# Performance work log

Hardware: AMD Instinct MI355X
Metric: run time of the kernel (lower is better)

The kernel has to match this reference:

```python
import jax, jax.numpy as jnp
import numpy as np

B, N, C = 4, 2048, 320
H, D = 5, 64            # heads, dim_head
INNER = H * D           # 320


def setup_inputs() -> dict:
    key = jax.random.key(0)
    ks = jax.random.split(key, 7)
    x = jax.random.normal(ks[0], (B, N, C), dtype=jnp.float32)
    edge = jax.random.uniform(ks[1], (B, N, 1), dtype=jnp.float32)
    s = 1.0 / np.sqrt(C)
    Wq = jax.random.normal(ks[2], (C, INNER), dtype=jnp.float32) * s
    Wk = jax.random.normal(ks[3], (C, INNER), dtype=jnp.float32) * s
    Wv = jax.random.normal(ks[4], (C, INNER), dtype=jnp.float32) * s
    Wo = jax.random.normal(ks[5], (INNER, C), dtype=jnp.float32) * (1.0 / np.sqrt(INNER))
    bo = jnp.zeros((C,), dtype=jnp.float32)
    return {"x": x, "edge": edge, "Wq": Wq, "Wk": Wk, "Wv": Wv, "Wo": Wo, "bo": bo}


def _split_heads(t):
    # 'b n (h d) -> (b h) n d'  (batch-major, head-minor)
    b, n, _ = t.shape
    return t.reshape(b, n, H, D).transpose(0, 2, 1, 3).reshape(b * H, n, D)


def reference(x, edge, Wq, Wk, Wv, Wo, bo):
    scale = D ** -0.5
    q = _split_heads(x @ Wq).astype(jnp.float32)   # (B*H, N, D)
    k = _split_heads(x @ Wk).astype(jnp.float32)
    v = _split_heads(x @ Wv)

    sim = jnp.einsum('bid,bjd->bij', q, k) * scale  # (B*H, N, N)

    # torch: edge.repeat(h, 1, 1) -> batch-minor tiling; index i uses edge[i % B]
    edge_rep = jnp.tile(edge, (H, 1, 1))            # (H*B, N, 1)
    edge_matrix = edge_rep * edge_rep.transpose(0, 2, 1)  # outer product (H*B, N, N)

    sim = jax.nn.softmax(sim * edge_matrix, axis=-1)
    out = jnp.einsum('bij,bjd->bid', sim, v)        # (B*H, N, D)

    # '(b h) n d -> b n (h d)'
    out = out.reshape(B, H, N, D).transpose(0, 2, 1, 3).reshape(B, N, INNER)
    return out @ Wo + bo
```

## Files before the change

### kernel.cpp

```cpp
#include <hip/hip_runtime.h>
#include <hip/hip_bf16.h>
#include <math.h>


typedef short bf16x8 __attribute__((ext_vector_type(8)));
typedef float f32x4 __attribute__((ext_vector_type(4)));

static __device__ __forceinline__ ushort f2bf(float f) {
  union { float f; unsigned u; } v; v.f = f;
  unsigned r = (v.u + 0x7fffu + ((v.u >> 16) & 1u)) >> 16;
  return (ushort)r;
}
static __device__ __forceinline__ float fexp2(float x) {
#if __has_builtin(__builtin_amdgcn_exp2f)
  return __builtin_amdgcn_exp2f(x);
#else
  return exp2f(x);
#endif
}
static __device__ __forceinline__ f32x4 mfma32(bf16x8 a, bf16x8 b, f32x4 c) {
  return __builtin_amdgcn_mfma_f32_16x16x32_bf16(a, b, c, 0, 0, 0);
}

#define GLD_LDS16(gsrc, ldst)                                                  \
  __builtin_amdgcn_global_load_lds(                                            \
      (const __attribute__((address_space(1))) unsigned int*)(gsrc),           \
      (__attribute__((address_space(3))) unsigned int*)(ldst), 16, 0, 0)

__global__ __launch_bounds__(256) void prep_kernel(
    const float* __restrict__ x,
    const float* __restrict__ Wq, const float* __restrict__ Wk,
    const float* __restrict__ Wv, const float* __restrict__ Wo,
    ushort* __restrict__ xb, ushort* __restrict__ wt)
{
  const int w = blockIdx.x;
  if (w < 2560) {
    const int t = threadIdx.x;
    const int mt2 = w / 5;
    const int kc = (w % 5) * 2 + (t >> 7);
    const int f = (t & 127) * 4;
    const int qq = f >> 7, mm = (f >> 3) & 15, e0 = f & 7;
    float4 v = *reinterpret_cast<const float4*>(
        x + (size_t)(mt2 * 16 + mm) * 320 + kc * 32 + qq * 8 + e0);
    ushort4 o = { f2bf(v.x), f2bf(v.y), f2bf(v.z), f2bf(v.w) };
    *reinterpret_cast<ushort4*>(xb + (size_t)(mt2 * 10 + kc) * 512 + f) = o;
  } else {
    const int w2 = w - 2560;
    const int nt2 = w2 % 20, kc = (w2 / 20) % 10, z = w2 / 200;
    const float* W = z == 0 ? Wq : z == 1 ? Wk : z == 2 ? Wv : Wo;
    const int f = threadIdx.x * 2;
    const int qq = f >> 7, nn = (f >> 3) & 15, e0 = f & 7;
    const int k = kc * 32 + qq * 8 + e0, n = nt2 * 16 + nn;
    float v0 = W[(size_t)k * 320 + n];
    float v1 = W[(size_t)(k + 1) * 320 + n];
    ushort2 o = { f2bf(v0), f2bf(v1) };
    *reinterpret_cast<ushort2*>(
        wt + (size_t)z * 102400 + (size_t)(nt2 * 10 + kc) * 512 + f) = o;
  }
}

__global__ __launch_bounds__(256, 3) void qkv_gemm(
    const ushort* __restrict__ xb, const float* __restrict__ edge,
    const ushort* __restrict__ wt,
    ushort* __restrict__ qp, ushort* __restrict__ kS, ushort* __restrict__ vS)
{
  const int w = blockIdx.x;
  const int s = (w & 7) * 60 + (w >> 3);
  const int mg = s / 15, zh = s % 15;
  const int z = zh / 5, h = zh % 5;
  const int wave = threadIdx.x >> 6, lane = threadIdx.x & 63;
  const int m16 = lane & 15, quad = lane >> 4;
  const int m0 = mg * 256 + wave * 64;
  const ushort* atile = xb + (size_t)(m0 >> 4) * 5120 + lane * 8;
  const ushort* btile = wt + (size_t)z * 102400 + (size_t)(h * 4) * 5120 + lane * 8;

  f32x4 acc[4][4];
#pragma unroll
  for (int i = 0; i < 4; ++i)
#pragma unroll
    for (int ns = 0; ns < 4; ++ns) acc[i][ns] = (f32x4){0.f, 0.f, 0.f, 0.f};

#pragma unroll
  for (int kc = 0; kc < 10; ++kc) {
    bf16x8 af[4], bf[4];
#pragma unroll
    for (int i = 0; i < 4; ++i)
      af[i] = *reinterpret_cast<const bf16x8*>(atile + (i * 10 + kc) * 512);
#pragma unroll
    for (int ns = 0; ns < 4; ++ns)
      bf[ns] = *reinterpret_cast<const bf16x8*>(btile + (ns * 10 + kc) * 512);
    if (z == 2) {
#pragma unroll
      for (int i = 0; i < 4; ++i)
#pragma unroll
        for (int ns = 0; ns < 4; ++ns)
          acc[i][ns] = mfma32(af[i], bf[ns], acc[i][ns]);
    } else {
#pragma unroll
      for (int i = 0; i < 4; ++i)
#pragma unroll
        for (int ns = 0; ns < 4; ++ns)
          acc[i][ns] = mfma32(bf[ns], af[i], acc[i][ns]);
    }
  }

  const float QSCALE = 0.18033688011112042f;
  const int b = m0 >> 11;
  const int bh = b * 5 + h;
  const float* eb = edge + (size_t)((b + h) & 3) * 2048;
  const int nwb = m0 & 2047;

  if (z == 0) {
#pragma unroll
    for (int i = 0; i < 4; ++i) {
      const int n = nwb + i * 16 + m16;
      const float e = eb[n] * QSCALE;
      ushort* dst = qp + ((size_t)bh * 2048 + n) * 64 + quad * 4;
#pragma unroll
      for (int ns = 0; ns < 4; ++ns) {
        ushort4 o = { f2bf(acc[i][ns][0] * e), f2bf(acc[i][ns][1] * e),
                      f2bf(acc[i][ns][2] * e), f2bf(acc[i][ns][3] * e) };
        *reinterpret_cast<ushort4*>(dst + ns * 16) = o;
      }
    }
  } else if (z == 1) {
#pragma unroll
    for (int i = 0; i < 4; ++i) {
      const int j = nwb + i * 16 + m16;
      const float e = eb[j];
      const size_t base = (size_t)bh * 131072 +
                          (size_t)((m0 >> 4) + i & 127) * 1024;
#pragma unroll
      for (int ns = 0; ns < 4; ++ns) {
        size_t a0 = base + (ns >> 1) * 512 +
                    ((((ns * 2 + (quad >> 1)) & 3) * 16 + m16)) * 8 +
                    (quad & 1) * 4;
        ushort4 o = { f2bf(acc[i][ns][0] * e), f2bf(acc[i][ns][1] * e),
                      f2bf(acc[i][ns][2] * e), f2bf(acc[i][ns][3] * e) };
        *reinterpret_cast<ushort4*>(kS + a0) = o;
      }
    }
  } else {
    const int jb = nwb >> 6;
#pragma unroll
    for (int i = 0; i < 4; ++i) {
      const int kb = i >> 1, e4 = (i & 1) * 4;
#pragma unroll
      for (int ns = 0; ns < 4; ++ns) {
        ushort4 o = { f2bf(acc[i][ns][0]), f2bf(acc[i][ns][1]),
                      f2bf(acc[i][ns][2]), f2bf(acc[i][ns][3]) };
        size_t addr = (size_t)bh * 131072 + (size_t)ns * 32768 +
                      (size_t)jb * 1024 + kb * 512 +
                      (quad * 16 + m16) * 8 + e4;
        *reinterpret_cast<ushort4*>(vS + addr) = o;
      }
    }
  }
}

__global__ __launch_bounds__(256, 4) void attn_kernel(
    const ushort* __restrict__ qp, const ushort* __restrict__ kS,
    const ushort* __restrict__ vS, ushort* __restrict__ ao)
{
  __shared__ ushort sm[16384];
  const int w = blockIdx.x;
  const int s = (w & 7) * 80 + (w >> 3);
  const int bh = s >> 5, qt = s & 31;
  const int b = bh / 5, h = bh % 5;
  const int wave = threadIdx.x >> 6, lane = threadIdx.x & 63;
  const int m16 = lane & 15, quad = lane >> 4;
  const int q0 = qt * 64;

  bf16x8 qf[2];
  {
    const ushort* qrow = qp + ((size_t)bh * 2048 + q0 + wave * 16 + m16) * 64;
    qf[0] = *reinterpret_cast<const bf16x8*>(qrow + quad * 8);
    qf[1] = *reinterpret_cast<const bf16x8*>(qrow + 32 + quad * 8);
  }

  const ushort* kbase = kS + (size_t)bh * 131072;
  const ushort* vbase = vS + (size_t)bh * 131072;

  f32x4 oacc[4];
  float rs = 0.f;
#pragma unroll
  for (int dt = 0; dt < 4; ++dt) oacc[dt] = (f32x4){0.f, 0.f, 0.f, 0.f};

  auto stage = [&](int jt, int buf) {
    const ushort* ks = kbase + (size_t)jt * 4096 + wave * 1024 + lane * 8;
    const ushort* vs = vbase + (size_t)wave * 32768 + (size_t)jt * 1024 + lane * 8;
    ushort* dk = &sm[buf * 8192 + wave * 1024];
    ushort* dv = &sm[buf * 8192 + 4096 + wave * 1024];
#pragma unroll
    for (int is = 0; is < 2; ++is) {
      GLD_LDS16(ks + is * 512, dk + is * 512);
      GLD_LDS16(vs + is * 512, dv + is * 512);
    }
  };

  stage(0, 0);
  __syncthreads();

  int cur = 0;
  for (int jt = 0; jt < 32; ++jt) {
    if (jt < 31) stage(jt + 1, cur ^ 1);
    const ushort* kb0 = &sm[cur * 8192];
    const ushort* vb0 = &sm[cur * 8192 + 4096];
#pragma unroll
    for (int uu = 0; uu < 2; ++uu) {
      bf16x8 kf[2][2], vf[4];
#pragma unroll
      for (int ss = 0; ss < 2; ++ss)
#pragma unroll
        for (int hf = 0; hf < 2; ++hf)
          kf[ss][hf] = *reinterpret_cast<const bf16x8*>(
              kb0 + uu * 2048 + ss * 1024 + hf * 512 + lane * 8);
#pragma unroll
      for (int dt = 0; dt < 4; ++dt)
        vf[dt] = *reinterpret_cast<const bf16x8*>(
            vb0 + dt * 1024 + uu * 512 + lane * 8);

      f32x4 st0 = (f32x4){0.f, 0.f, 0.f, 0.f};
      f32x4 st1 = (f32x4){0.f, 0.f, 0.f, 0.f};
      st0 = mfma32(kf[0][0], qf[0], st0);
      st0 = mfma32(kf[0][1], qf[1], st0);
      st1 = mfma32(kf[1][0], qf[0], st1);
      st1 = mfma32(kf[1][1], qf[1], st1);
      unsigned b0 = __float_as_uint(fexp2(st0[0]));
      unsigned b1 = __float_as_uint(fexp2(st0[1]));
      unsigned b2 = __float_as_uint(fexp2(st0[2]));
      unsigned b3 = __float_as_uint(fexp2(st0[3]));
      unsigned b4 = __float_as_uint(fexp2(st1[0]));
      unsigned b5 = __float_as_uint(fexp2(st1[1]));
      unsigned b6 = __float_as_uint(fexp2(st1[2]));
      unsigned b7 = __float_as_uint(fexp2(st1[3]));
      float t0 = __uint_as_float(b0 & 0xffff0000u);
      float t1 = __uint_as_float(b1 & 0xffff0000u);
      float t2 = __uint_as_float(b2 & 0xffff0000u);
      float t3 = __uint_as_float(b3 & 0xffff0000u);
      float t4 = __uint_as_float(b4 & 0xffff0000u);
      float t5 = __uint_as_float(b5 & 0xffff0000u);
      float t6 = __uint_as_float(b6 & 0xffff0000u);
      float t7 = __uint_as_float(b7 & 0xffff0000u);
      rs += ((t0 + t1) + (t2 + t3)) + ((t4 + t5) + (t6 + t7));
      union { unsigned u[4]; bf16x8 v; } pk;
      pk.u[0] = __builtin_amdgcn_perm(b1, b0, 0x07060302u);
      pk.u[1] = __builtin_amdgcn_perm(b3, b2, 0x07060302u);
      pk.u[2] = __builtin_amdgcn_perm(b5, b4, 0x07060302u);
      pk.u[3] = __builtin_amdgcn_perm(b7, b6, 0x07060302u);
#pragma unroll
      for (int dt = 0; dt < 4; ++dt)
        oacc[dt] = mfma32(vf[dt], pk.v, oacc[dt]);
    }
    __syncthreads();
    cur ^= 1;
  }

  rs += __shfl_xor(rs, 16, 64);
  rs += __shfl_xor(rs, 32, 64);
  const float inv = 1.0f / rs;

  const int mt2 = b * 128 + qt * 4 + wave;
#pragma unroll
  for (int dt = 0; dt < 4; ++dt) {
    f32x4 a = oacc[dt];
    unsigned r0 = f2bf(a[0] * inv), r1 = f2bf(a[1] * inv);
    unsigned r2 = f2bf(a[2] * inv), r3 = f2bf(a[3] * inv);
    uint2 ww;
    ww.x = r0 | (r1 << 16);
    ww.y = r2 | (r3 << 16);
    size_t addr = (size_t)(mt2 * 10 + h * 2 + (dt >> 1)) * 512 +
                  ((((dt & 1) * 2 + (quad >> 1)) * 16 + m16)) * 8 +
                  (quad & 1) * 4;
    *reinterpret_cast<uint2*>(ao + addr) = ww;
  }
}

__global__ __launch_bounds__(256, 3) void oproj_gemm(
    const ushort* __restrict__ ao, const ushort* __restrict__ wt,
    const float* __restrict__ bo, float* __restrict__ out)
{
  const int w = blockIdx.x;
  const int s = (w & 7) * 40 + (w >> 3);
  const int mg = s / 5, ct = s % 5;
  const int wave = threadIdx.x >> 6, lane = threadIdx.x & 63;
  const int m16 = lane & 15, quad = lane >> 4;
  const int m0 = mg * 128 + wave * 32;
  const int n0 = ct * 64;
  const ushort* atile = ao + (size_t)(m0 >> 4) * 5120 + lane * 8;
  const ushort* btile = wt + (size_t)3 * 102400 + (size_t)(ct * 4) * 5120 + lane * 8;

  f32x4 acc[2][4];
#pragma unroll
  for (int i = 0; i < 2; ++i)
#pragma unroll
    for (int ns = 0; ns < 4; ++ns) acc[i][ns] = (f32x4){0.f, 0.f, 0.f, 0.f};

#pragma unroll
  for (int kc = 0; kc < 10; ++kc) {
    bf16x8 af[2], bf[4];
#pragma unroll
    for (int i = 0; i < 2; ++i)
      af[i] = *reinterpret_cast<const bf16x8*>(atile + (i * 10 + kc) * 512);
#pragma unroll
    for (int ns = 0; ns < 4; ++ns)
      bf[ns] = *reinterpret_cast<const bf16x8*>(btile + (ns * 10 + kc) * 512);
#pragma unroll
    for (int i = 0; i < 2; ++i)
#pragma unroll
      for (int ns = 0; ns < 4; ++ns)
        acc[i][ns] = mfma32(bf[ns], af[i], acc[i][ns]);
  }

  float4 bb[4];
#pragma unroll
  for (int ns = 0; ns < 4; ++ns)
    bb[ns] = *reinterpret_cast<const float4*>(bo + n0 + ns * 16 + quad * 4);
#pragma unroll
  for (int i = 0; i < 2; ++i) {
    const int mrow = m0 + i * 16 + m16;
#pragma unroll
    for (int ns = 0; ns < 4; ++ns) {
      float4 o;
      o.x = acc[i][ns][0] + bb[ns].x;
      o.y = acc[i][ns][1] + bb[ns].y;
      o.z = acc[i][ns][2] + bb[ns].z;
      o.w = acc[i][ns][3] + bb[ns].w;
      *reinterpret_cast<float4*>(
          out + (size_t)mrow * 320 + n0 + ns * 16 + quad * 4) = o;
    }
  }
}

extern "C" void kernel_launch(void* const* d_in, const int* in_sizes, int n_in,
                              void* d_out, int out_size, void* d_ws, size_t ws_size,
                              hipStream_t stream) {
  const float* x    = (const float*)d_in[0];
  const float* edge = (const float*)d_in[1];
  const float* Wq   = (const float*)d_in[2];
  const float* Wk   = (const float*)d_in[3];
  const float* Wv   = (const float*)d_in[4];
  const float* Wo   = (const float*)d_in[5];
  const float* bo   = (const float*)d_in[6];
  float* out = (float*)d_out;

  ushort* xb = (ushort*)d_ws;
  ushort* wt = xb + (size_t)8192 * 320;
  ushort* qp = wt + (size_t)4 * 320 * 320;
  ushort* kS = qp + (size_t)20 * 2048 * 64;
  ushort* vS = kS + (size_t)20 * 2048 * 64;
  ushort* ao = vS + (size_t)20 * 2048 * 64;

  prep_kernel<<<3360, 256, 0, stream>>>(x, Wq, Wk, Wv, Wo, xb, wt);
  qkv_gemm<<<480, 256, 0, stream>>>(xb, edge, wt, qp, kS, vS);
  attn_kernel<<<640, 256, 0, stream>>>(qp, kS, vS, ao);
  oproj_gemm<<<320, 256, 0, stream>>>(ao, wt, bo, out);
}
```

Before: 128.1 us.

## Process two query tiles per wave to reuse staged K/V across more queries

Each wave in the attention kernel now computes two 16-row query subtiles, so a block covers 128 queries instead of 64 and the grid is halved. K/V tiles loaded into shared memory and the K/V fragments read from it are reused for twice the query work. This cuts global K/V traffic and LDS reads per query, at the cost of more accumulator registers and fewer blocks, which may unbalance CU occupancy.

```diff
diff --git a/kernel.cpp b/kernel.cpp
--- a/kernel.cpp
+++ b/kernel.cpp
@@ -164,27 +164,31 @@
 {
   __shared__ ushort sm[16384];
   const int w = blockIdx.x;
-  const int s = (w & 7) * 80 + (w >> 3);
-  const int bh = s >> 5, qt = s & 31;
+  const int s = (w & 7) * 40 + (w >> 3);
+  const int bh = s >> 4, qt = s & 15;
   const int b = bh / 5, h = bh % 5;
   const int wave = threadIdx.x >> 6, lane = threadIdx.x & 63;
   const int m16 = lane & 15, quad = lane >> 4;
-  const int q0 = qt * 64;
-
-  bf16x8 qf[2];
-  {
-    const ushort* qrow = qp + ((size_t)bh * 2048 + q0 + wave * 16 + m16) * 64;
-    qf[0] = *reinterpret_cast<const bf16x8*>(qrow + quad * 8);
-    qf[1] = *reinterpret_cast<const bf16x8*>(qrow + 32 + quad * 8);
+  const int q0 = qt * 128;
+
+  bf16x8 qf[2][2];
+#pragma unroll
+  for (int qt2 = 0; qt2 < 2; ++qt2) {
+    const ushort* qrow =
+        qp + ((size_t)bh * 2048 + q0 + wave * 32 + qt2 * 16 + m16) * 64;
+    qf[qt2][0] = *reinterpret_cast<const bf16x8*>(qrow + quad * 8);
+    qf[qt2][1] = *reinterpret_cast<const bf16x8*>(qrow + 32 + quad * 8);
   }
 
   const ushort* kbase = kS + (size_t)bh * 131072;
   const ushort* vbase = vS + (size_t)bh * 131072;
 
-  f32x4 oacc[4];
-  float rs = 0.f;
-#pragma unroll
-  for (int dt = 0; dt < 4; ++dt) oacc[dt] = (f32x4){0.f, 0.f, 0.f, 0.f};
+  f32x4 oacc[2][4];
+  float rs[2] = {0.f, 0.f};
+#pragma unroll
+  for (int qt2 = 0; qt2 < 2; ++qt2)
+#pragma unroll
+    for (int dt = 0; dt < 4; ++dt) oacc[qt2][dt] = (f32x4){0.f, 0.f, 0.f, 0.f};
 
   auto stage = [&](int jt, int buf) {
     const ushort* ks = kbase + (size_t)jt * 4096 + wave * 1024 + lane * 8;
@@ -220,59 +224,66 @@
         vf[dt] = *reinterpret_cast<const bf16x8*>(
             vb0 + dt * 1024 + uu * 512 + lane * 8);
 
-      f32x4 st0 = (f32x4){0.f, 0.f, 0.f, 0.f};
-      f32x4 st1 = (f32x4){0.f, 0.f, 0.f, 0.f};
-      st0 = mfma32(kf[0][0], qf[0], st0);
-      st0 = mfma32(kf[0][1], qf[1], st0);
-      st1 = mfma32(kf[1][0], qf[0], st1);
-      st1 = mfma32(kf[1][1], qf[1], st1);
-      unsigned b0 = __float_as_uint(fexp2(st0[0]));
-      unsigned b1 = __float_as_uint(fexp2(st0[1]));
-      unsigned b2 = __float_as_uint(fexp2(st0[2]));
-      unsigned b3 = __float_as_uint(fexp2(st0[3]));
-      unsigned b4 = __float_as_uint(fexp2(st1[0]));
-      unsigned b5 = __float_as_uint(fexp2(st1[1]));
-      unsigned b6 = __float_as_uint(fexp2(st1[2]));
-      unsigned b7 = __float_as_uint(fexp2(st1[3]));
-      float t0 = __uint_as_float(b0 & 0xffff0000u);
-      float t1 = __uint_as_float(b1 & 0xffff0000u);
-      float t2 = __uint_as_float(b2 & 0xffff0000u);
-      float t3 = __uint_as_float(b3 & 0xffff0000u);
-      float t4 = __uint_as_float(b4 & 0xffff0000u);
-      float t5 = __uint_as_float(b5 & 0xffff0000u);
-      float t6 = __uint_as_float(b6 & 0xffff0000u);
-      float t7 = __uint_as_float(b7 & 0xffff0000u);
-      rs += ((t0 + t1) + (t2 + t3)) + ((t4 + t5) + (t6 + t7));
-      union { unsigned u[4]; bf16x8 v; } pk;
-      pk.u[0] = __builtin_amdgcn_perm(b1, b0, 0x07060302u);
-      pk.u[1] = __builtin_amdgcn_perm(b3, b2, 0x07060302u);
-      pk.u[2] = __builtin_amdgcn_perm(b5, b4, 0x07060302u);
-      pk.u[3] = __builtin_amdgcn_perm(b7, b6, 0x07060302u);
-#pragma unroll
-      for (int dt = 0; dt < 4; ++dt)
-        oacc[dt] = mfma32(vf[dt], pk.v, oacc[dt]);
+#pragma unroll
+      for (int qt2 = 0; qt2 < 2; ++qt2) {
+        f32x4 st0 = (f32x4){0.f, 0.f, 0.f, 0.f};
+        f32x4 st1 = (f32x4){0.f, 0.f, 0.f, 0.f};
+        st0 = mfma32(kf[0][0], qf[qt2][0], st0);
+        st0 = mfma32(kf[0][1], qf[qt2][1], st0);
+        st1 = mfma32(kf[1][0], qf[qt2][0], st1);
+        st1 = mfma32(kf[1][1], qf[qt2][1], st1);
+        unsigned b0 = __float_as_uint(fexp2(st0[0]));
+        unsigned b1 = __float_as_uint(fexp2(st0[1]));
+        unsigned b2 = __float_as_uint(fexp2(st0[2]));
+        unsigned b3 = __float_as_uint(fexp2(st0[3]));
+        unsigned b4 = __float_as_uint(fexp2(st1[0]));
+        unsigned b5 = __float_as_uint(fexp2(st1[1]));
+        unsigned b6 = __float_as_uint(fexp2(st1[2]));
+        unsigned b7 = __float_as_uint(fexp2(st1[3]));
+        float t0 = __uint_as_float(b0 & 0xffff0000u);
+        float t1 = __uint_as_float(b1 & 0xffff0000u);
+        float t2 = __uint_as_float(b2 & 0xffff0000u);
+        float t3 = __uint_as_float(b3 & 0xffff0000u);
+        float t4 = __uint_as_float(b4 & 0xffff0000u);
+        float t5 = __uint_as_float(b5 & 0xffff0000u);
+        float t6 = __uint_as_float(b6 & 0xffff0000u);
+        float t7 = __uint_as_float(b7 & 0xffff0000u);
+        rs[qt2] += ((t0 + t1) + (t2 + t3)) + ((t4 + t5) + (t6 + t7));
+        union { unsigned u[4]; bf16x8 v; } pk;
+        pk.u[0] = __builtin_amdgcn_perm(b1, b0, 0x07060302u);
+        pk.u[1] = __builtin_amdgcn_perm(b3, b2, 0x07060302u);
+        pk.u[2] = __builtin_amdgcn_perm(b5, b4, 0x07060302u);
+        pk.u[3] = __builtin_amdgcn_perm(b7, b6, 0x07060302u);
+#pragma unroll
+        for (int dt = 0; dt < 4; ++dt)
+          oacc[qt2][dt] = mfma32(vf[dt], pk.v, oacc[qt2][dt]);
+      }
     }
     __syncthreads();
     cur ^= 1;
   }
 
-  rs += __shfl_xor(rs, 16, 64);
-  rs += __shfl_xor(rs, 32, 64);
-  const float inv = 1.0f / rs;
-
-  const int mt2 = b * 128 + qt * 4 + wave;
-#pragma unroll
-  for (int dt = 0; dt < 4; ++dt) {
-    f32x4 a = oacc[dt];
-    unsigned r0 = f2bf(a[0] * inv), r1 = f2bf(a[1] * inv);
-    unsigned r2 = f2bf(a[2] * inv), r3 = f2bf(a[3] * inv);
-    uint2 ww;
-    ww.x = r0 | (r1 << 16);
-    ww.y = r2 | (r3 << 16);
-    size_t addr = (size_t)(mt2 * 10 + h * 2 + (dt >> 1)) * 512 +
-                  ((((dt & 1) * 2 + (quad >> 1)) * 16 + m16)) * 8 +
-                  (quad & 1) * 4;
-    *reinterpret_cast<uint2*>(ao + addr) = ww;
+#pragma unroll
+  for (int qt2 = 0; qt2 < 2; ++qt2) {
+    float r = rs[qt2];
+    r += __shfl_xor(r, 16, 64);
+    r += __shfl_xor(r, 32, 64);
+    const float inv = 1.0f / r;
+
+    const int mt2 = b * 128 + qt * 8 + wave * 2 + qt2;
+#pragma unroll
+    for (int dt = 0; dt < 4; ++dt) {
+      f32x4 a = oacc[qt2][dt];
+      unsigned r0 = f2bf(a[0] * inv), r1 = f2bf(a[1] * inv);
+      unsigned r2 = f2bf(a[2] * inv), r3 = f2bf(a[3] * inv);
+      uint2 ww;
+      ww.x = r0 | (r1 << 16);
+      ww.y = r2 | (r3 << 16);
+      size_t addr = (size_t)(mt2 * 10 + h * 2 + (dt >> 1)) * 512 +
+                    ((((dt & 1) * 2 + (quad >> 1)) * 16 + m16)) * 8 +
+                    (quad & 1) * 4;
+      *reinterpret_cast<uint2*>(ao + addr) = ww;
+    }
   }
 }
 
@@ -353,6 +364,6 @@
 
   prep_kernel<<<3360, 256, 0, stream>>>(x, Wq, Wk, Wv, Wo, xb, wt);
   qkv_gemm<<<480, 256, 0, stream>>>(xb, edge, wt, qp, kS, vS);
-  attn_kernel<<<640, 256, 0, stream>>>(qp, kS, vS, ao);
+  attn_kernel<<<320, 256, 0, stream>>>(qp, kS, vS, ao);
   oproj_gemm<<<320, 256, 0, stream>>>(ao, wt, bo, out);
 }
```

New measurement: 148.7 us. 1.16x slower.
